# Performance work log

Hardware: AMD Instinct MI355X
Metric: run time of the kernel (lower is better)

The kernel has to match this reference:

```python
import jax, jax.numpy as jnp
import numpy as np

B, N, D, H, QV = 8, 1024, 64, 4, 32
C = 2 * D + 1          # combined_dim = 129
K = C // 8             # per-head qk dim = 16
M_PER = 512
M = B * M_PER
NEG = -9e15


def setup_inputs() -> dict:
    key = jax.random.key(0)
    ks = jax.random.split(key, 24)
    s = 0.05
    x = jax.random.normal(ks[0], (B, N, D + 1), jnp.float32)
    h = jax.random.normal(ks[1], (B, N, D), jnp.float32)
    query_vectors = jax.random.normal(ks[2], (M, QV), jnp.float32)
    adj = jax.random.randint(ks[3], (N, N), 0, 2, jnp.int32)
    # unique observed nodes per graph (mimics torch.where on an obs mask)
    perm = jax.vmap(lambda k: jax.random.permutation(k, N))(jax.random.split(ks[4], B))
    nodes_n = perm[:, :M_PER].reshape(-1).astype(jnp.int32)
    nodes_b = jnp.repeat(jnp.arange(B, dtype=jnp.int32), M_PER)
    # per-head attention projections, stacked over heads
    Wq = jax.random.normal(ks[5], (H, C, K), jnp.float32) * s
    bq = jax.random.normal(ks[6], (H, K), jnp.float32) * s
    Wk = jax.random.normal(ks[7], (H, C, K), jnp.float32) * s
    bk = jax.random.normal(ks[8], (H, K), jnp.float32) * s
    Wv = jax.random.normal(ks[9], (H, C, C), jnp.float32) * s
    bv = jax.random.normal(ks[10], (H, C), jnp.float32) * s
    # attentionMLP: Linear(H*C, C) -> ReLU -> Linear(C, C)
    W1 = jax.random.normal(ks[11], (H * C, C), jnp.float32) * s
    b1 = jax.random.normal(ks[12], (C,), jnp.float32) * s
    W2 = jax.random.normal(ks[13], (C, C), jnp.float32) * s
    b2 = jax.random.normal(ks[14], (C,), jnp.float32) * s
    # MLP_Param hypernetwork tensors: W[qvd, in=C, out=D], b[qvd, D]
    Wr = jax.random.normal(ks[15], (QV, C, D), jnp.float32) * s
    br = jax.random.normal(ks[16], (QV, D), jnp.float32) * s
    Wu = jax.random.normal(ks[17], (QV, C, D), jnp.float32) * s
    bu = jax.random.normal(ks[18], (QV, D), jnp.float32) * s
    Wc = jax.random.normal(ks[19], (QV, C, D), jnp.float32) * s
    bc = jax.random.normal(ks[20], (QV, D), jnp.float32) * s
    return dict(x=x, h=h, query_vectors=query_vectors, adj=adj,
                nodes_b=nodes_b, nodes_n=nodes_n,
                Wq=Wq, bq=bq, Wk=Wk, bk=bk, Wv=Wv, bv=bv,
                W1=W1, b1=b1, W2=W2, b2=b2,
                Wr=Wr, br=br, Wu=Wu, bu=bu, Wc=Wc, bc=bc)


def _mlp_param(sel, qv, W, b):
    # hypernetwork: per-node generated linear layer
    Wn = jnp.einsum('md,dio->mio', qv, W)   # [M, C, D]
    bn = qv @ b                              # [M, D]
    return jnp.einsum('mi,mio->mo', sel, Wn) + bn


def reference(x, h, query_vectors, adj, nodes_b, nodes_n,
              Wq, bq, Wk, bk, Wv, bv, W1, b1, W2, b2,
              Wr, br, Wu, bu, Wc, bc):
    combined = jnp.concatenate([x, h], axis=-1)                      # [B,N,C]
    q = jnp.einsum('bnc,hck->hbnk', combined, Wq) + bq[:, None, None, :]
    k = jnp.einsum('bnc,hck->hbnk', combined, Wk) + bk[:, None, None, :]
    v = jnp.einsum('bnc,hcd->hbnd', combined, Wv) + bv[:, None, None, :]
    scores = jnp.einsum('hbnk,hbmk->hbnm', q, k) / jnp.sqrt(jnp.float32(K))
    scores = jax.nn.leaky_relu(scores, 0.2)
    scores = jnp.where(adj == 0, NEG, scores)                        # [N,N] broadcast
    attn = jax.nn.softmax(scores, axis=-1)                           # [H,B,N,N]
    hp = jnp.einsum('hbnm,hbmd->hbnd', attn, v)                      # [H,B,N,C]
    # permute(1,2,0,3).reshape -> concat heads per node
    attn_cat = jnp.transpose(hp, (1, 2, 0, 3)).reshape(B, N, H * C)
    mlp_out = jax.nn.relu(attn_cat @ W1 + b1) @ W2 + b2              # [B,N,C]
    combined = mlp_out + combined                                    # skip connection
    sel = combined[nodes_b, nodes_n]                                 # [M,C]
    r = jax.nn.sigmoid(_mlp_param(sel, query_vectors, Wr, br))       # [M,D]
    u = jax.nn.sigmoid(_mlp_param(sel, query_vectors, Wu, bu))       # [M,D]
    h = h.at[nodes_b, nodes_n].set(r * h[nodes_b, nodes_n])
    combined_new = jnp.concatenate([x, h], axis=-1)
    cand = jnp.tanh(_mlp_param(combined_new[nodes_b, nodes_n], query_vectors, Wc, bc))
    new_h = (1.0 - u) * h[nodes_b, nodes_n] + u * cand               # [M,D]
    return new_h
```

## Files before the change

### kernel.cpp

```cpp
#include <hip/hip_runtime.h>

#define DEVINL __device__ __forceinline__

typedef unsigned short ushort_t;
typedef unsigned long long u64;
typedef __attribute__((ext_vector_type(8))) short short8;
typedef __attribute__((ext_vector_type(8))) unsigned short ushort8;
typedef __attribute__((ext_vector_type(4))) float f32x4;

constexpr int B_ = 8, N_ = 1024, D_ = 64, H_ = 4, QV_ = 32;
constexpr int C_ = 129, K_ = 16, M_ = 4096;
constexpr int CP = 132;
constexpr int NG = B_ * N_;
constexpr int CBS = 160;
constexpr int VTN = 144;
constexpr int KT = 4256;
constexpr int NKT = 133;
constexpr int ZS = 8;
constexpr int HPS = 544;
constexpr int NCH = NG / 32;

constexpr size_t o_cb    = 0;
constexpr size_t o_qb    = o_cb  + (size_t)NG * CBS / 2;
constexpr size_t o_kb    = o_qb  + (size_t)H_ * NG * 16 / 2;
constexpr size_t o_adjb  = o_kb  + (size_t)H_ * NG * 16 / 2;
constexpr size_t o_wqk   = o_adjb + 32768;
constexpr size_t o_wvt   = o_wqk + (size_t)H_ * 32 * CBS / 2;
constexpr size_t o_vT    = o_wvt + (size_t)H_ * VTN * CBS / 2;
constexpr size_t o_hpb   = o_vT  + (size_t)H_ * VTN * NG / 2;
constexpr size_t o_cpost = o_hpb + (size_t)M_ * HPS / 2;
constexpr size_t o_W1T   = o_cpost + (size_t)M_ * CP;
constexpr size_t o_W2T   = o_W1T + (size_t)144 * HPS / 2;
constexpr size_t o_wtru  = o_W2T + (size_t)144 * 160 / 2;
constexpr size_t o_wtc   = o_wtru + (size_t)128 * KT / 2;
constexpr size_t o_A     = o_wtc + (size_t)64 * KT / 2;
constexpr size_t o_pru   = o_A + (size_t)M_ * KT / 2;
constexpr size_t o_pc2   = o_pru + (size_t)ZS * M_ * 128;

constexpr int SEG0 = NG * CBS;
constexpr int SEG1 = SEG0 + H_ * 32 * CBS;
constexpr int SEG2 = SEG1 + H_ * VTN * CBS;
constexpr int SEG3 = SEG2 + 144 * HPS;
constexpr int SEG4 = SEG3 + 144 * 160;
constexpr int SEG5 = SEG4 + 192 * KT;
constexpr int SEG6 = SEG5 + 1024 * 16 * 64;

DEVINL float4 ld4(const float* p) { return *reinterpret_cast<const float4*>(p); }
DEVINL void st4(float* p, float4 v) { *reinterpret_cast<float4*>(p) = v; }
DEVINL ushort_t f2bf(float f) {
    unsigned int u = __float_as_uint(f);
    u += 0x7FFFu + ((u >> 16) & 1u);
    return (ushort_t)(u >> 16);
}

__global__ void k_prep(const float* __restrict__ x, const float* __restrict__ h,
                       const float* __restrict__ Wq, const float* __restrict__ bq,
                       const float* __restrict__ Wk, const float* __restrict__ bk,
                       const float* __restrict__ Wv, const float* __restrict__ bv,
                       const float* __restrict__ W1, const float* __restrict__ W2,
                       const float* __restrict__ Wr, const float* __restrict__ br,
                       const float* __restrict__ Wu, const float* __restrict__ bu,
                       const float* __restrict__ Wc, const float* __restrict__ bc,
                       const int* __restrict__ adj,
                       ushort_t* __restrict__ cb, ushort_t* __restrict__ wqk,
                       ushort_t* __restrict__ wvt, ushort_t* __restrict__ W1T,
                       ushort_t* __restrict__ W2T, ushort_t* __restrict__ wtru,
                       ushort_t* __restrict__ wtc, u64* __restrict__ ab) {
    int idx = blockIdx.x * 256 + threadIdx.x;
    if (idx < SEG0) {
        int g = idx / CBS, kk = idx - g * CBS;
        float v;
        if (kk < 65) v = x[g * 65 + kk];
        else if (kk < 129) v = h[g * 64 + (kk - 65)];
        else if (kk == 129) v = 1.0f;
        else v = 0.f;
        cb[((size_t)(kk >> 5) * NG + g) * 32 + (kk & 31)] = f2bf(v);
    } else if (idx < SEG1) {
        int j = idx - SEG0;
        int hh = j / (32 * CBS); int rem = j - hh * 32 * CBS;
        int o = rem / CBS, kk = rem - o * CBS;
        float v = 0.f;
        if (o < 16) {
            if (kk < 129) v = Wq[(size_t)(hh * C_ + kk) * K_ + o];
            else if (kk == 129) v = bq[hh * K_ + o];
        } else {
            int o2 = o - 16;
            if (kk < 129) v = Wk[(size_t)(hh * C_ + kk) * K_ + o2];
            else if (kk == 129) v = bk[hh * K_ + o2];
        }
        wqk[((size_t)(hh * 5 + (kk >> 5)) * 32 + o) * 32 + (kk & 31)] = f2bf(v);
    } else if (idx < SEG2) {
        int j = idx - SEG1;
        int hh = j / (VTN * CBS); int rem = j - hh * VTN * CBS;
        int n = rem / CBS, kk = rem - n * CBS;
        float v = 0.f;
        if (n < C_) {
            if (kk < 129) v = Wv[(size_t)(hh * C_ + kk) * C_ + n];
            else if (kk == 129) v = bv[hh * C_ + n];
        }
        wvt[((size_t)(hh * 5 + (kk >> 5)) * 144 + n) * 32 + (kk & 31)] = f2bf(v);
    } else if (idx < SEG3) {
        int j = idx - SEG2;
        int o = j / HPS, k = j - o * HPS;
        float v = (o < C_ && k < 516) ? W1[(size_t)k * C_ + o] : 0.f;
        W1T[((size_t)(k >> 5) * 144 + o) * 32 + (k & 31)] = f2bf(v);
    } else if (idx < SEG4) {
        int j = idx - SEG3;
        int o = j / 160, k = j - o * 160;
        float v = (o < C_ && k < C_) ? W2[(size_t)k * C_ + o] : 0.f;
        W2T[((size_t)(k >> 5) * 144 + o) * 32 + (k & 31)] = f2bf(v);
    } else if (idx < SEG5) {
        int j = idx - SEG4;
        int row = j / KT, k = j - row * KT;
        float v;
        if (k >= 4224) {
            int d = k - 4224;
            if (row < 64) v = br[d * 64 + row];
            else if (row < 128) v = bu[d * 64 + row - 64];
            else v = bc[d * 64 + row - 128];
        } else {
            int d = k / 132, i = k - d * 132;
            if (i >= 129) v = 0.f;
            else if (row < 64) v = Wr[(size_t)(d * 129 + i) * 64 + row];
            else if (row < 128) v = Wu[(size_t)(d * 129 + i) * 64 + row - 64];
            else v = Wc[(size_t)(d * 129 + i) * 64 + row - 128];
        }
        int kt = k >> 5, kj = k & 31;
        if (row < 128) wtru[((size_t)kt * 128 + row) * 32 + kj] = f2bf(v);
        else wtc[((size_t)kt * 64 + (row - 128)) * 32 + kj] = f2bf(v);
    } else if (idx < SEG6) {
        int j = idx - SEG5;
        int word = j >> 6, lane = j & 63;
        int row = word >> 4, wj = word & 15;
        u64 m = __ballot(adj[(size_t)row * N_ + wj * 64 + lane] != 0);
        if (lane == 0) ab[word] = m;
    }
}

__global__ __launch_bounds__(256) void k_qkv(
    const ushort_t* __restrict__ cb, const ushort_t* __restrict__ wqk,
    const ushort_t* __restrict__ wvt,
    ushort_t* __restrict__ qbo, ushort_t* __restrict__ kbo, ushort_t* __restrict__ vTg) {
    const int t = threadIdx.x;
    const int g0 = blockIdx.x * 16;
    const int hh = blockIdx.y;
    const int lane = t & 63, w = t >> 6;
    const int am = lane & 15, aq = lane >> 4;
    short8 cbf[5];
#pragma unroll
    for (int kt = 0; kt < 5; ++kt)
        cbf[kt] = *reinterpret_cast<const short8*>(&cb[((size_t)kt * NG + g0 + am) * 32 + aq * 8]);
#pragma unroll
    for (int s = 0; s < 3; ++s) {
        int u = w + 4 * s;
        if (u >= 11) break;
        f32x4 acc = f32x4{0.f, 0.f, 0.f, 0.f};
        if (u < 2) {
#pragma unroll
            for (int kt = 0; kt < 5; ++kt) {
                short8 bf = *reinterpret_cast<const short8*>(
                    &wqk[((size_t)(hh * 5 + kt) * 32 + u * 16 + am) * 32 + aq * 8]);
                acc = __builtin_amdgcn_mfma_f32_16x16x32_bf16(cbf[kt], bf, acc, 0, 0, 0);
            }
            ushort_t* dst = u ? kbo : qbo;
#pragma unroll
            for (int i = 0; i < 4; ++i)
                dst[(size_t)(hh * NG + g0 + aq * 4 + i) * 16 + am] = f2bf(acc[i]);
        } else {
            int vt = u - 2;
#pragma unroll
            for (int kt = 0; kt < 5; ++kt) {
                short8 af = *reinterpret_cast<const short8*>(
                    &wvt[((size_t)(hh * 5 + kt) * 144 + vt * 16 + am) * 32 + aq * 8]);
                acc = __builtin_amdgcn_mfma_f32_16x16x32_bf16(af, cbf[kt], acc, 0, 0, 0);
            }
            const int g = g0 + am;
#pragma unroll
            for (int i = 0; i < 4; ++i) {
                int feat = vt * 16 + aq * 4 + i;
                vTg[(((size_t)hh * NCH + (g >> 5)) * 144 + feat) * 32 + (g & 31)] = f2bf(acc[i]);
            }
        }
    }
}

__global__ __launch_bounds__(256) void k_attn(
    const ushort_t* __restrict__ qb, const ushort_t* __restrict__ kb,
    const ushort_t* __restrict__ vTg, const u64* __restrict__ adjb,
    const int* __restrict__ nodes_b, const int* __restrict__ nodes_n,
    ushort_t* __restrict__ hpb) {
    __shared__ u64 Msk[16][16];
    __shared__ alignas(16) ushort_t Pb[4][16 * 72];
    __shared__ float Ored[3][16 * 144];
    __shared__ float Lpart[4][16];
    __shared__ float Linv[16];
    __shared__ int Nrow[16];
    const int t = threadIdx.x;
    const int bi = blockIdx.x;
    const int mx = ((bi & 7) << 5) + (bi >> 3);
    const int m0 = mx * 16;
    const int hh = blockIdx.y;
    const int b = nodes_b[m0];
    if (t < 16) Nrow[t] = nodes_n[m0 + t];
    __syncthreads();
    { int r = t >> 4, wj = t & 15; Msk[r][wj] = adjb[Nrow[r] * 16 + wj]; }
    const int lane = t & 63, w = t >> 6;
    const int am = lane & 15, aq = lane >> 4;
    short8 qf = short8{0, 0, 0, 0, 0, 0, 0, 0};
    if (aq < 2)
        qf = *reinterpret_cast<const short8*>(&qb[(size_t)(hh * NG + b * N_ + Nrow[am]) * 16 + aq * 8]);
    __syncthreads();
    ushort_t* Pw = Pb[w];
    const ushort_t* kbase = kb + ((size_t)hh * NG + b * N_) * 16;
    const ushort_t* vbase = vTg + ((size_t)hh * NCH + b * 32) * 144 * 32;
    f32x4 accv[9];
#pragma unroll
    for (int j = 0; j < 9; ++j) accv[j] = f32x4{0.f, 0.f, 0.f, 0.f};
    float lsum[4] = {0.f, 0.f, 0.f, 0.f};

    for (int ti = 0; ti < 4; ++ti) {
        const int tile = w + 4 * ti;
        const int c0 = tile * 64;
        u64 mrow[4];
#pragma unroll
        for (int i = 0; i < 4; ++i) mrow[i] = Msk[aq * 4 + i][tile];
#pragma unroll
        for (int nt = 0; nt < 4; ++nt) {
            int col = c0 + nt * 16 + am;
            short8 bf = short8{0, 0, 0, 0, 0, 0, 0, 0};
            if (aq < 2)
                bf = *reinterpret_cast<const short8*>(&kbase[(size_t)col * 16 + aq * 8]);
            f32x4 sv = __builtin_amdgcn_mfma_f32_16x16x32_bf16(qf, bf, f32x4{0.f, 0.f, 0.f, 0.f}, 0, 0, 0);
#pragma unroll
            for (int i = 0; i < 4; ++i) {
                float s = sv[i] * 0.25f;
                s = (s >= 0.f) ? s : 0.2f * s;
                float p = ((mrow[i] >> (nt * 16 + am)) & 1ull) ? __expf(s) : 0.f;
                lsum[i] += p;
                Pw[(aq * 4 + i) * 72 + nt * 16 + am] = f2bf(p);
            }
        }
#pragma unroll
        for (int kh = 0; kh < 2; ++kh) {
            short8 af = *reinterpret_cast<const short8*>(&Pw[am * 72 + kh * 32 + aq * 8]);
            const ushort_t* vch = vbase + ((size_t)((c0 >> 5) + kh) * 144) * 32;
#pragma unroll
            for (int nt = 0; nt < 9; ++nt) {
                short8 bfr = *reinterpret_cast<const short8*>(
                    &vch[(size_t)(nt * 16 + am) * 32 + aq * 8]);
                accv[nt] = __builtin_amdgcn_mfma_f32_16x16x32_bf16(af, bfr, accv[nt], 0, 0, 0);
            }
        }
    }
#pragma unroll
    for (int i = 0; i < 4; ++i) {
        float v = lsum[i];
        v += __shfl_xor(v, 1); v += __shfl_xor(v, 2);
        v += __shfl_xor(v, 4); v += __shfl_xor(v, 8);
        if (am == 0) Lpart[w][aq * 4 + i] = v;
    }
    if (w > 0) {
#pragma unroll
        for (int nt = 0; nt < 9; ++nt)
#pragma unroll
            for (int i = 0; i < 4; ++i)
                Ored[w - 1][(aq * 4 + i) * 144 + nt * 16 + am] = accv[nt][i];
    }
    __syncthreads();
    if (w == 0) {
        if (t < 16) {
            float s = Lpart[0][t] + Lpart[1][t] + Lpart[2][t] + Lpart[3][t];
            Linv[t] = (s > 0.f) ? 1.f / s : 0.f;
        }
#pragma unroll
        for (int nt = 0; nt < 9; ++nt) {
            int col = nt * 16 + am;
            if (col < C_) {
                int k = hh * C_ + col;
#pragma unroll
                for (int i = 0; i < 4; ++i) {
                    int row = aq * 4 + i;
                    float val = accv[nt][i] + Ored[0][row * 144 + col]
                              + Ored[1][row * 144 + col] + Ored[2][row * 144 + col];
                    hpb[((size_t)(k >> 5) * M_ + m0 + row) * 32 + (k & 31)] = f2bf(val * Linv[row]);
                }
            }
        }
    }
    if (hh == 3) {
        for (int idx = t; idx < 16 * 28; idx += 256) {
            int rr = idx / 28, cc = 516 + (idx - rr * 28);
            hpb[((size_t)(cc >> 5) * M_ + m0 + rr) * 32 + (cc & 31)] = 0;
        }
    }
}

__global__ __launch_bounds__(256) void k_mlp(
    const ushort_t* __restrict__ hpb,
    const ushort_t* __restrict__ W1T, const float* __restrict__ b1,
    const ushort_t* __restrict__ W2T, const float* __restrict__ b2,
    const float* __restrict__ x, const float* __restrict__ h,
    const int* __restrict__ nb, const int* __restrict__ nn,
    float* __restrict__ cpost) {
    __shared__ alignas(16) ushort_t Hs[16 * 168];
    const int t = threadIdx.x;
    const int m0 = blockIdx.x * 16;
    const int lane = t & 63, w = t >> 6;
    const int am = lane & 15, aq = lane >> 4;
    f32x4 acc[3];
#pragma unroll
    for (int j = 0; j < 3; ++j) acc[j] = f32x4{0.f, 0.f, 0.f, 0.f};
    for (int kt = 0; kt < 17; ++kt) {
        short8 af = *reinterpret_cast<const short8*>(&hpb[((size_t)kt * M_ + m0 + am) * 32 + aq * 8]);
#pragma unroll
        for (int j = 0; j < 3; ++j) {
            int nt = w + 4 * j;
            if (nt < 9) {
                short8 bf = *reinterpret_cast<const short8*>(
                    &W1T[((size_t)kt * 144 + nt * 16 + am) * 32 + aq * 8]);
                acc[j] = __builtin_amdgcn_mfma_f32_16x16x32_bf16(af, bf, acc[j], 0, 0, 0);
            }
        }
    }
#pragma unroll
    for (int j = 0; j < 3; ++j) {
        int nt = w + 4 * j;
        if (nt < 9) {
            int col = nt * 16 + am;
            float bb = (col < C_) ? b1[col] : 0.f;
#pragma unroll
            for (int i = 0; i < 4; ++i) {
                int row = aq * 4 + i;
                float v = (col < C_) ? fmaxf(acc[j][i] + bb, 0.f) : 0.f;
                Hs[row * 168 + col] = f2bf(v);
            }
        }
    }
    { int row = t >> 4, cc = 144 + (t & 15); Hs[row * 168 + cc] = 0; }
    __syncthreads();
    f32x4 acc2[3];
#pragma unroll
    for (int j = 0; j < 3; ++j) acc2[j] = f32x4{0.f, 0.f, 0.f, 0.f};
    for (int kt = 0; kt < 5; ++kt) {
        short8 af = *reinterpret_cast<const short8*>(&Hs[am * 168 + kt * 32 + aq * 8]);
#pragma unroll
        for (int j = 0; j < 3; ++j) {
            int nt = w + 4 * j;
            if (nt < 9) {
                short8 bf = *reinterpret_cast<const short8*>(
                    &W2T[((size_t)kt * 144 + nt * 16 + am) * 32 + aq * 8]);
                acc2[j] = __builtin_amdgcn_mfma_f32_16x16x32_bf16(af, bf, acc2[j], 0, 0, 0);
            }
        }
    }
#pragma unroll
    for (int j = 0; j < 3; ++j) {
        int nt = w + 4 * j;
        if (nt < 9) {
            int col = nt * 16 + am;
            if (col < C_) {
                float bb = b2[col];
#pragma unroll
                for (int i = 0; i < 4; ++i) {
                    int m = m0 + aq * 4 + i;
                    int b = nb[m], n = nn[m];
                    float sk = (col < 65) ? x[(b * N_ + n) * 65 + col]
                                          : h[(b * N_ + n) * D_ + (col - 65)];
                    cpost[(size_t)m * CP + col] = acc2[j][i] + bb + sk;
                }
            }
        }
    }
    if (t < 48) {
        int rr = t / 3, cc = 129 + (t - (t / 3) * 3);
        cpost[(size_t)(m0 + rr) * CP + cc] = 0.f;
    }
}

__global__ __launch_bounds__(256) void k_arow(const float* __restrict__ src,
                                              const float* __restrict__ qv,
                                              ushort_t* __restrict__ A) {
    __shared__ float sq[CP];
    __shared__ float qs[QV_];
    const int t = threadIdx.x;
    const int m = blockIdx.x;
    if (t < CP) sq[t] = src[(size_t)m * CP + t];
    if (t >= 224) qs[t - 224] = qv[m * QV_ + (t - 224)];
    __syncthreads();
    for (int k = t; k < 4224; k += 256) {
        int d = k / 132, i = k - d * 132;
        A[((size_t)(k >> 5) * M_ + m) * 32 + (k & 31)] = f2bf(qs[d] * sq[i]);
    }
    if (t < QV_) A[((size_t)132 * M_ + m) * 32 + t] = f2bf(qs[t]);
}

__global__ __launch_bounds__(256) void k_arow2(const float* __restrict__ x,
                                               const float* __restrict__ h,
                                               const int* __restrict__ nb,
                                               const int* __restrict__ nn,
                                               const float* __restrict__ pru,
                                               const float* __restrict__ qv,
                                               ushort_t* __restrict__ A) {
    __shared__ float sq[132];
    __shared__ float qs[QV_];
    const int t = threadIdx.x;
    const int m = blockIdx.x;
    const int b = nb[m], n = nn[m];
    if (t < 65) sq[t] = x[(b * N_ + n) * 65 + t];
    else if (t < 129) {
        int o = t - 65;
        const size_t S = (size_t)M_ * 128;
        size_t base = (size_t)m * 128 + o;
        float s = 0.f;
#pragma unroll
        for (int z = 0; z < ZS; ++z) s += pru[z * S + base];
        float rv = 1.f / (1.f + __expf(-s));
        sq[t] = rv * h[(b * N_ + n) * D_ + o];
    } else if (t < 132) sq[t] = 0.f;
    if (t >= 224) qs[t - 224] = qv[m * QV_ + (t - 224)];
    __syncthreads();
    for (int k = t; k < 4224; k += 256) {
        int d = k / 132, i = k - d * 132;
        A[((size_t)(k >> 5) * M_ + m) * 32 + (k & 31)] = f2bf(qs[d] * sq[i]);
    }
    if (t < QV_) A[((size_t)132 * M_ + m) * 32 + t] = f2bf(qs[t]);
}

template<int NN>
__global__ __launch_bounds__(256) void k_gemm(const ushort_t* __restrict__ A,
                                              const ushort_t* __restrict__ WT,
                                              float* __restrict__ part) {
    const int t = threadIdx.x;
    const int m0 = blockIdx.x * 32;
    const int z = blockIdx.y;
    const int lane = t & 63, w = t >> 6;
    const int am = lane & 15, aq = lane >> 4;
    constexpr int NTpW = NN / 64;
    const int ktb = z * 17;
    const int kte = (ktb + 17 < NKT) ? ktb + 17 : NKT;
    f32x4 acc[2][NTpW];
#pragma unroll
    for (int r2 = 0; r2 < 2; ++r2)
#pragma unroll
        for (int j = 0; j < NTpW; ++j) acc[r2][j] = f32x4{0.f, 0.f, 0.f, 0.f};
    for (int kt = ktb; kt < kte; ++kt) {
        const ushort_t* Ab = A + ((size_t)kt * M_ + m0) * 32 + aq * 8;
        short8 a0 = *reinterpret_cast<const short8*>(Ab + am * 32);
        short8 a1 = *reinterpret_cast<const short8*>(Ab + (am + 16) * 32);
        const ushort_t* Bb = WT + (size_t)kt * NN * 32 + am * 32 + aq * 8;
#pragma unroll
        for (int j = 0; j < NTpW; ++j) {
            int nt = w + 4 * j;
            short8 bf = *reinterpret_cast<const short8*>(Bb + nt * 16 * 32);
            acc[0][j] = __builtin_amdgcn_mfma_f32_16x16x32_bf16(a0, bf, acc[0][j], 0, 0, 0);
            acc[1][j] = __builtin_amdgcn_mfma_f32_16x16x32_bf16(a1, bf, acc[1][j], 0, 0, 0);
        }
    }
#pragma unroll
    for (int j = 0; j < NTpW; ++j) {
        int n = (w + 4 * j) * 16 + am;
#pragma unroll
        for (int r2 = 0; r2 < 2; ++r2)
#pragma unroll
            for (int i = 0; i < 4; ++i) {
                int m = m0 + r2 * 16 + aq * 4 + i;
                part[((size_t)z * M_ + m) * NN + n] = acc[r2][j][i];
            }
    }
}

__global__ void k_final(const float* __restrict__ pru, const float* __restrict__ pc,
                        const float* __restrict__ h,
                        const int* __restrict__ nb, const int* __restrict__ nn,
                        float* __restrict__ out) {
    int idx = blockIdx.x * 256 + threadIdx.x;
    if (idx >= M_ * D_) return;
    int m = idx >> 6, o = idx & 63;
    const size_t Su = (size_t)M_ * 128;
    size_t br_ = (size_t)m * 128 + o;
    size_t bu = br_ + 64;
    float sr = 0.f, su = 0.f;
#pragma unroll
    for (int z = 0; z < ZS; ++z) { sr += pru[z * Su + br_]; su += pru[z * Su + bu]; }
    float rv = 1.f / (1.f + __expf(-sr));
    float uv = 1.f / (1.f + __expf(-su));
    const size_t Sc = (size_t)M_ * 64;
    size_t bcx = (size_t)m * 64 + o;
    float sc = 0.f;
#pragma unroll
    for (int z = 0; z < ZS; ++z) sc += pc[z * Sc + bcx];
    float cand = tanhf(sc);
    int b = nb[m], n = nn[m];
    float hn = rv * h[(b * N_ + n) * D_ + o];
    out[idx] = (1.f - uv) * hn + uv * cand;
}

extern "C" void kernel_launch(void* const* d_in, const int* in_sizes, int n_in,
                              void* d_out, int out_size, void* d_ws, size_t ws_size,
                              hipStream_t stream) {
    const float* x   = (const float*)d_in[0];
    const float* h   = (const float*)d_in[1];
    const float* qv  = (const float*)d_in[2];
    const int*   adj = (const int*)d_in[3];
    const int*   nb  = (const int*)d_in[4];
    const int*   nn  = (const int*)d_in[5];
    const float* Wq  = (const float*)d_in[6];
    const float* bq  = (const float*)d_in[7];
    const float* Wk  = (const float*)d_in[8];
    const float* bk  = (const float*)d_in[9];
    const float* Wv  = (const float*)d_in[10];
    const float* bv  = (const float*)d_in[11];
    const float* W1  = (const float*)d_in[12];
    const float* b1  = (const float*)d_in[13];
    const float* W2  = (const float*)d_in[14];
    const float* b2  = (const float*)d_in[15];
    const float* Wr  = (const float*)d_in[16];
    const float* br  = (const float*)d_in[17];
    const float* Wu  = (const float*)d_in[18];
    const float* bu  = (const float*)d_in[19];
    const float* Wc  = (const float*)d_in[20];
    const float* bc  = (const float*)d_in[21];
    float* ws = (float*)d_ws;
    float* out = (float*)d_out;

    ushort_t* cb   = (ushort_t*)(ws + o_cb);
    ushort_t* qb   = (ushort_t*)(ws + o_qb);
    ushort_t* kb   = (ushort_t*)(ws + o_kb);
    u64*      ab   = (u64*)(ws + o_adjb);
    ushort_t* wqk  = (ushort_t*)(ws + o_wqk);
    ushort_t* wvt  = (ushort_t*)(ws + o_wvt);
    ushort_t* vTg  = (ushort_t*)(ws + o_vT);
    ushort_t* hpb  = (ushort_t*)(ws + o_hpb);
    float* cpost = ws + o_cpost;
    ushort_t* W1T  = (ushort_t*)(ws + o_W1T);
    ushort_t* W2T  = (ushort_t*)(ws + o_W2T);
    ushort_t* wtru = (ushort_t*)(ws + o_wtru);
    ushort_t* wtc  = (ushort_t*)(ws + o_wtc);
    ushort_t* Abuf = (ushort_t*)(ws + o_A);
    float* pru   = ws + o_pru;
    float* pc    = ws + o_pc2;

    k_prep<<<(SEG6 + 255) / 256, 256, 0, stream>>>(
        x, h, Wq, bq, Wk, bk, Wv, bv, W1, W2, Wr, br, Wu, bu, Wc, bc, adj,
        cb, wqk, wvt, W1T, W2T, wtru, wtc, ab);
    k_qkv<<<dim3(NG / 16, H_), 256, 0, stream>>>(cb, wqk, wvt, qb, kb, vTg);
    k_attn<<<dim3(M_ / 16, H_), 256, 0, stream>>>(qb, kb, vTg, ab, nb, nn, hpb);
    k_mlp<<<M_ / 16, 256, 0, stream>>>(hpb, W1T, b1, W2T, b2, x, h, nb, nn, cpost);
    k_arow<<<M_, 256, 0, stream>>>(cpost, qv, Abuf);
    k_gemm<128><<<dim3(M_ / 32, ZS), 256, 0, stream>>>(Abuf, wtru, pru);
    k_arow2<<<M_, 256, 0, stream>>>(x, h, nb, nn, pru, qv, Abuf);
    k_gemm<64><<<dim3(M_ / 32, ZS), 256, 0, stream>>>(Abuf, wtc, pc);
    k_final<<<(M_ * D_ + 255) / 256, 256, 0, stream>>>(pru, pc, h, nb, nn, out);
}
```

Before: 258.0 us.

## Split attention PV matmul by output columns across warps instead of key tiles

```diff
diff --git a/kernel.cpp b/kernel.cpp
--- a/kernel.cpp
+++ b/kernel.cpp
@@ -19,6 +19,7 @@
 constexpr int ZS = 8;
 constexpr int HPS = 544;
 constexpr int NCH = NG / 32;
+constexpr int PBS = 1096;
 
 constexpr size_t o_cb    = 0;
 constexpr size_t o_qb    = o_cb  + (size_t)NG * CBS / 2;
@@ -190,10 +191,8 @@
     const int* __restrict__ nodes_b, const int* __restrict__ nodes_n,
     ushort_t* __restrict__ hpb) {
     __shared__ u64 Msk[16][16];
-    __shared__ alignas(16) ushort_t Pb[4][16 * 72];
-    __shared__ float Ored[3][16 * 144];
+    __shared__ alignas(16) ushort_t Pball[16 * PBS];
     __shared__ float Lpart[4][16];
-    __shared__ float Linv[16];
     __shared__ int Nrow[16];
     const int t = threadIdx.x;
     const int bi = blockIdx.x;
@@ -210,14 +209,11 @@
     if (aq < 2)
         qf = *reinterpret_cast<const short8*>(&qb[(size_t)(hh * NG + b * N_ + Nrow[am]) * 16 + aq * 8]);
     __syncthreads();
-    ushort_t* Pw = Pb[w];
     const ushort_t* kbase = kb + ((size_t)hh * NG + b * N_) * 16;
     const ushort_t* vbase = vTg + ((size_t)hh * NCH + b * 32) * 144 * 32;
-    f32x4 accv[9];
-#pragma unroll
-    for (int j = 0; j < 9; ++j) accv[j] = f32x4{0.f, 0.f, 0.f, 0.f};
     float lsum[4] = {0.f, 0.f, 0.f, 0.f};
 
+#pragma unroll
     for (int ti = 0; ti < 4; ++ti) {
         const int tile = w + 4 * ti;
         const int c0 = tile * 64;
@@ -237,18 +233,7 @@
                 s = (s >= 0.f) ? s : 0.2f * s;
                 float p = ((mrow[i] >> (nt * 16 + am)) & 1ull) ? __expf(s) : 0.f;
                 lsum[i] += p;
-                Pw[(aq * 4 + i) * 72 + nt * 16 + am] = f2bf(p);
-            }
-        }
-#pragma unroll
-        for (int kh = 0; kh < 2; ++kh) {
-            short8 af = *reinterpret_cast<const short8*>(&Pw[am * 72 + kh * 32 + aq * 8]);
-            const ushort_t* vch = vbase + ((size_t)((c0 >> 5) + kh) * 144) * 32;
-#pragma unroll
-            for (int nt = 0; nt < 9; ++nt) {
-                short8 bfr = *reinterpret_cast<const short8*>(
-                    &vch[(size_t)(nt * 16 + am) * 32 + aq * 8]);
-                accv[nt] = __builtin_amdgcn_mfma_f32_16x16x32_bf16(af, bfr, accv[nt], 0, 0, 0);
+                Pball[(aq * 4 + i) * PBS + col] = f2bf(p);
             }
         }
     }
@@ -259,30 +244,41 @@
         v += __shfl_xor(v, 4); v += __shfl_xor(v, 8);
         if (am == 0) Lpart[w][aq * 4 + i] = v;
     }
-    if (w > 0) {
-#pragma unroll
-        for (int nt = 0; nt < 9; ++nt)
-#pragma unroll
-            for (int i = 0; i < 4; ++i)
-                Ored[w - 1][(aq * 4 + i) * 144 + nt * 16 + am] = accv[nt][i];
-    }
     __syncthreads();
-    if (w == 0) {
-        if (t < 16) {
-            float s = Lpart[0][t] + Lpart[1][t] + Lpart[2][t] + Lpart[3][t];
-            Linv[t] = (s > 0.f) ? 1.f / s : 0.f;
-        }
-#pragma unroll
-        for (int nt = 0; nt < 9; ++nt) {
+    float linv[4];
+#pragma unroll
+    for (int i = 0; i < 4; ++i) {
+        int row = aq * 4 + i;
+        float s = Lpart[0][row] + Lpart[1][row] + Lpart[2][row] + Lpart[3][row];
+        linv[i] = (s > 0.f) ? 1.f / s : 0.f;
+    }
+
+    f32x4 acc[3];
+#pragma unroll
+    for (int j = 0; j < 3; ++j) acc[j] = f32x4{0.f, 0.f, 0.f, 0.f};
+    for (int ck = 0; ck < 32; ++ck) {
+        short8 af = *reinterpret_cast<const short8*>(&Pball[am * PBS + ck * 32 + aq * 8]);
+        const ushort_t* vch = vbase + (size_t)ck * 144 * 32;
+#pragma unroll
+        for (int j = 0; j < 3; ++j) {
+            int nt = w + 4 * j;
+            if (nt < 9) {
+                short8 bf = *reinterpret_cast<const short8*>(&vch[(size_t)(nt * 16 + am) * 32 + aq * 8]);
+                acc[j] = __builtin_amdgcn_mfma_f32_16x16x32_bf16(af, bf, acc[j], 0, 0, 0);
+            }
+        }
+    }
+#pragma unroll
+    for (int j = 0; j < 3; ++j) {
+        int nt = w + 4 * j;
+        if (nt < 9) {
             int col = nt * 16 + am;
             if (col < C_) {
                 int k = hh * C_ + col;
 #pragma unroll
                 for (int i = 0; i < 4; ++i) {
                     int row = aq * 4 + i;
-                    float val = accv[nt][i] + Ored[0][row * 144 + col]
-                              + Ored[1][row * 144 + col] + Ored[2][row * 144 + col];
-                    hpb[((size_t)(k >> 5) * M_ + m0 + row) * 32 + (k & 31)] = f2bf(val * Linv[row]);
+                    hpb[((size_t)(k >> 5) * M_ + m0 + row) * 32 + (k & 31)] = f2bf(acc[j][i] * linv[i]);
                 }
             }
         }
```

After: 256.2 us. About the same (-0.7%).
